# Kernel optimization log

Hardware: AMD Instinct MI355X
Metric: run time of the kernel (lower is better)

The kernel has to match this reference:

```python
import jax, jax.numpy as jnp
import numpy as np

EMBED_DIM = 768
SCALE = float(np.sqrt(EMBED_DIM / 9.0))


def setup_inputs() -> dict:
    key = jax.random.key(0)
    ks = jax.random.split(key, 7)
    D = EMBED_DIM
    s = 1.0 / np.sqrt(D)
    x = jax.random.normal(ks[0], (8, 2048, D), dtype=jnp.float32)
    Wq = jax.random.uniform(ks[1], (D, D), jnp.float32, -s, s)
    bq = jax.random.uniform(ks[2], (D,), jnp.float32, -s, s)
    Wk = jax.random.uniform(ks[3], (D, D), jnp.float32, -s, s)
    bk = jax.random.uniform(ks[4], (D,), jnp.float32, -s, s)
    Wv = jax.random.uniform(ks[5], (D, D), jnp.float32, -s, s)
    bv = jax.random.uniform(ks[6], (D,), jnp.float32, -s, s)
    return {"x": x, "Wq": Wq, "bq": bq, "Wk": Wk, "bk": bk, "Wv": Wv, "bv": bv}


def reference(x, Wq, bq, Wk, bk, Wv, bv):
    # nn.Linear: y = x @ W^T + b
    Q = jnp.einsum('bnd,ed->bne', x, Wq) + bq
    K = jnp.einsum('bnd,ed->bne', x, Wk) + bk
    V = jnp.einsum('bnd,ed->bne', x, Wv) + bv
    scores = jnp.einsum('bqd,bkd->bqk', Q, K) / SCALE  # [B, Nq, Nk]
    # NOTE: softmax over the QUERY axis (dim=-2), per the original module
    weights = jax.nn.softmax(scores, axis=-2)
    out = jnp.einsum('bqk,bkd->bqd', weights, V)
    return out + x
```

## Files before the change

kernel.cpp:

```cpp
#include <hip/hip_runtime.h>
#include <stdint.h>

#define B_ 8
#define N_ 2048
#define D_ 768

typedef unsigned short u16;
typedef unsigned int u32;
typedef __attribute__((ext_vector_type(8))) short bf16x8;
typedef __attribute__((ext_vector_type(8))) unsigned short u16x8;
typedef __attribute__((ext_vector_type(4))) float f32x4;

static constexpr float INV_SCALE = 0.10825317547305482f;

__device__ __forceinline__ u16 f2bf(float f) {
  union { float f; unsigned u; } v; v.f = f;
  return (u16)((v.u + 0x7FFFu + ((v.u >> 16) & 1u)) >> 16);
}
__device__ __forceinline__ float bf2f(u16 h) {
  union { unsigned u; float f; } v; v.u = ((unsigned)h) << 16;
  return v.f;
}
__device__ __forceinline__ f32x4 mfma16(bf16x8 a, bf16x8 b, f32x4 c) {
  return __builtin_amdgcn_mfma_f32_16x16x32_bf16(a, b, c, 0, 0, 0);
}
__device__ __forceinline__ void gl_lds16(const void* g, void* l) {
  __builtin_amdgcn_global_load_lds(
      (const __attribute__((address_space(1))) u32*)g,
      (__attribute__((address_space(3))) u32*)l, 16, 0, 0);
}

__global__ __launch_bounds__(256) void cast_kernel(
    const float* __restrict__ x, const float* __restrict__ wq,
    const float* __restrict__ wk, const float* __restrict__ wv,
    u16* __restrict__ xb, u16* __restrict__ wqb,
    u16* __restrict__ wkb, u16* __restrict__ wvb) {
  const long NX = (long)B_ * N_ * D_;
  const long NW = (long)D_ * D_;
  long i = ((long)blockIdx.x * 256 + threadIdx.x) * 8;
  const float* src; u16* dst; long off;
  if (i < NX) { src = x; dst = xb; off = i; }
  else {
    long j = i - NX;
    int seg = (int)(j / NW);
    off = j - (long)seg * NW;
    src = seg == 0 ? wq : (seg == 1 ? wk : wv);
    dst = seg == 0 ? wqb : (seg == 1 ? wkb : wvb);
  }
  float4 a = *(const float4*)(src + off);
  float4 b = *(const float4*)(src + off + 4);
  u16x8 o;
  o[0]=f2bf(a.x); o[1]=f2bf(a.y); o[2]=f2bf(a.z); o[3]=f2bf(a.w);
  o[4]=f2bf(b.x); o[5]=f2bf(b.y); o[6]=f2bf(b.z); o[7]=f2bf(b.w);
  *(u16x8*)(dst + off) = o;
}

template<int NT, int NF>
__device__ __forceinline__ void gemm256(
    const u16* __restrict__ Ag, long lda,
    const u16* __restrict__ Bg, long ldb,
    f32x4 (&acc)[8][NF]) {
  __shared__ u16 Ab[2][16384];
  __shared__ u16 Bb[2][NF * 4096];
  const int t_ = threadIdx.x, l = t_ & 63, w = t_ >> 6;
  const int lr = l & 15, kq = l >> 4;
  const int wm = w >> 2, wn = w & 3;
  const int arow = wm * 128, brow = wn * (NF * 16);
  const int s_rowl = l >> 3;
  const int s_sl = (l & 7) ^ (l >> 3);
  auto STAGE_A = [&](u16* As, int kt) {
    #pragma unroll
    for (int j = 0; j < 4; ++j) {
      const int row = j * 64 + w * 8 + s_rowl;
      gl_lds16(Ag + (long)row * lda + kt * 64 + s_sl * 8,
               As + ((j * 8192 + w * 1024) >> 1));
    }
  };
  auto STAGE_B = [&](u16* Bs, int kt) {
    #pragma unroll
    for (int j = 0; j < NF; ++j) {
      const int row = j * 64 + w * 8 + s_rowl;
      gl_lds16(Bg + (long)row * ldb + kt * 64 + s_sl * 8,
               Bs + ((j * 8192 + w * 1024) >> 1));
    }
  };

#define TILE(XA, XB, YA, YB, kt, DOST)                                       \
  {                                                                          \
    if (DOST) {                                                              \
      STAGE_A(YA, (kt) + 1);                                                 \
      asm volatile("s_waitcnt vmcnt(4)" ::: "memory");                       \
    } else {                                                                 \
      asm volatile("s_waitcnt vmcnt(0)" ::: "memory");                       \
    }                                                                        \
    __builtin_amdgcn_s_barrier();                                            \
    asm volatile("" ::: "memory");                                           \
    bf16x8 bf[NF][2];                                                        \
    _Pragma("unroll")                                                        \
    for (int nf = 0; nf < NF; ++nf) {                                        \
      const int row = brow + nf * 16 + lr;                                   \
      _Pragma("unroll")                                                      \
      for (int ks = 0; ks < 2; ++ks)                                         \
        bf[nf][ks] = *(const bf16x8*)(XB + row * 64 +                        \
                        (((4 * ks + kq) ^ (lr & 7)) * 8));                   \
    }                                                                        \
    {                                                                        \
      bf16x8 af[4][2];                                                       \
      _Pragma("unroll")                                                      \
      for (int mf = 0; mf < 4; ++mf) {                                       \
        const int row = arow + mf * 16 + lr;                                 \
        _Pragma("unroll")                                                    \
        for (int ks = 0; ks < 2; ++ks)                                       \
          af[mf][ks] = *(const bf16x8*)(XA + row * 64 +                      \
                          (((4 * ks + kq) ^ (lr & 7)) * 8));                 \
      }                                                                      \
      __builtin_amdgcn_s_setprio(1);                                         \
      _Pragma("unroll")                                                      \
      for (int ks = 0; ks < 2; ++ks)                                         \
        _Pragma("unroll")                                                    \
        for (int mf = 0; mf < 4; ++mf)                                       \
          _Pragma("unroll")                                                  \
          for (int nf = 0; nf < NF; ++nf)                                    \
            acc[mf][nf] = mfma16(af[mf][ks], bf[nf][ks], acc[mf][nf]);       \
      __builtin_amdgcn_s_setprio(0);                                         \
    }                                                                        \
    if (DOST) STAGE_B(YB, (kt) + 1);                                         \
    {                                                                        \
      bf16x8 af[4][2];                                                       \
      _Pragma("unroll")                                                      \
      for (int mf = 0; mf < 4; ++mf) {                                       \
        const int row = arow + 64 + mf * 16 + lr;                            \
        _Pragma("unroll")                                                    \
        for (int ks = 0; ks < 2; ++ks)                                       \
          af[mf][ks] = *(const bf16x8*)(XA + row * 64 +                      \
                          (((4 * ks + kq) ^ (lr & 7)) * 8));                 \
      }                                                                      \
      __builtin_amdgcn_s_setprio(1);                                         \
      _Pragma("unroll")                                                      \
      for (int ks = 0; ks < 2; ++ks)                                         \
        _Pragma("unroll")                                                    \
        for (int mf = 0; mf < 4; ++mf)                                       \
          _Pragma("unroll")                                                  \
          for (int nf = 0; nf < NF; ++nf)                                    \
            acc[4 + mf][nf] = mfma16(af[mf][ks], bf[nf][ks], acc[4 + mf][nf]); \
      __builtin_amdgcn_s_setprio(0);                                         \
    }                                                                        \
    asm volatile("" ::: "memory");                                           \
    __builtin_amdgcn_s_barrier();                                            \
  }

  STAGE_A(Ab[0], 0);
  STAGE_B(Bb[0], 0);
  for (int t2 = 0; t2 < NT; t2 += 2) {
    TILE(Ab[0], Bb[0], Ab[1], Bb[1], t2, true)
    TILE(Ab[1], Bb[1], Ab[0], Bb[0], t2 + 1, (t2 + 2 < NT))
  }
#undef TILE
}

__global__ __launch_bounds__(512, 1) void qkv_gemm(
    const u16* __restrict__ xb,
    const u16* __restrict__ wq, const u16* __restrict__ wk, const u16* __restrict__ wv,
    const float* __restrict__ bq, const float* __restrict__ bk, const float* __restrict__ bv,
    u16* __restrict__ Qs, u16* __restrict__ Kb, u16* __restrict__ Vb) {
  const int lin = blockIdx.x;
  const int xcd = lin & 7, inner = lin >> 3;
  const int rt = xcd * 8 + (inner & 7);
  const int ct = inner >> 3;
  const int mat = ct >> 2;
  const u16* W = mat == 0 ? wq : (mat == 1 ? wk : wv);
  const float* bias = mat == 0 ? bq : (mat == 1 ? bk : bv);
  u16* out = mat == 0 ? Qs : (mat == 1 ? Kb : Vb);
  const float scl = mat == 0 ? INV_SCALE : 1.0f;
  const int rbase = rt * 256, cbase = (ct & 3) * 192;

  f32x4 acc[8][3] = {};
  gemm256<D_ / 64, 3>(xb + (long)rbase * D_, D_, W + (long)cbase * D_, D_, acc);

  const int l = threadIdx.x & 63, w = threadIdx.x >> 6;
  const int lr = l & 15, orow = (l >> 4) * 4;
  const int wm = w >> 2, wn = w & 3;
  #pragma unroll
  for (int mf = 0; mf < 8; ++mf)
    #pragma unroll
    for (int nf = 0; nf < 3; ++nf) {
      int col = cbase + wn * 48 + nf * 16 + lr;
      float bc = bias[col];
      #pragma unroll
      for (int r = 0; r < 4; ++r) {
        int row = rbase + wm * 128 + mf * 16 + orow + r;
        out[(long)row * D_ + col] = f2bf((acc[mf][nf][r] + bc) * scl);
      }
    }
}

__global__ __launch_bounds__(512, 1) void qk_exp(
    const u16* __restrict__ Qs, const u16* __restrict__ Kb,
    u16* __restrict__ P, float* __restrict__ denpart) {
  const int lin = blockIdx.x;
  const int b = lin & 7, inner = lin >> 3;
  const int kblk = inner & 7, qblk = inner >> 3;

  f32x4 acc[8][4] = {};
  gemm256<D_ / 64, 4>(Qs + ((long)b * N_ + qblk * 256) * D_, D_,
                      Kb + ((long)b * N_ + kblk * 256) * D_, D_, acc);

  const int tt = threadIdx.x, l = tt & 63, w = tt >> 6;
  const int lr = l & 15, orow = (l >> 4) * 4;
  const int wm = w >> 2, wn = w & 3;
  float csum[4] = {0.f, 0.f, 0.f, 0.f};
  #pragma unroll
  for (int mf = 0; mf < 8; ++mf)
    #pragma unroll
    for (int nf = 0; nf < 4; ++nf) {
      long kk = kblk * 256 + wn * 64 + nf * 16 + lr;
      #pragma unroll
      for (int r = 0; r < 4; ++r) {
        long q = qblk * 256 + wm * 128 + mf * 16 + orow + r;
        float e = __expf(acc[mf][nf][r]);
        u16 pe = f2bf(e);
        P[((long)b * N_ + q) * N_ + kk] = pe;
        csum[nf] += bf2f(pe);
      }
    }
  #pragma unroll
  for (int nf = 0; nf < 4; ++nf) {
    csum[nf] += __shfl_xor(csum[nf], 16);
    csum[nf] += __shfl_xor(csum[nf], 32);
  }
  if (l < 16) {
    #pragma unroll
    for (int nf = 0; nf < 4; ++nf)
      denpart[((long)(qblk * 2 + wm) * B_ + b) * N_ +
              kblk * 256 + wn * 64 + nf * 16 + l] = csum[nf];
  }
}

__global__ __launch_bounds__(256) void scale_transpose(
    const u16* __restrict__ Vb, const float* __restrict__ denpart,
    u16* __restrict__ VsT) {
  const int b = blockIdx.z, k0 = blockIdx.y * 64, d0 = blockIdx.x * 64;
  __shared__ float tile[64][65];
  __shared__ float invden[64];
  const int t = threadIdx.x;
  if (t < 64) {
    float s = 0.f;
    for (int qs = 0; qs < 16; ++qs)
      s += denpart[((long)qs * B_ + b) * N_ + k0 + t];
    invden[t] = 1.0f / s;
  }
  __syncthreads();
  #pragma unroll
  for (int h = 0; h < 2; ++h) {
    const int kl = (t >> 3) + h * 32;
    const int d8 = (t & 7) * 8;
    bf16x8 v = *(const bf16x8*)(Vb + ((long)b * N_ + k0 + kl) * D_ + d0 + d8);
    const float s = invden[kl];
    #pragma unroll
    for (int j = 0; j < 8; ++j)
      tile[d8 + j][kl] = bf2f((u16)v[j]) * s;
  }
  __syncthreads();
  #pragma unroll
  for (int h = 0; h < 2; ++h) {
    const int dl = (t >> 3) + h * 32;
    const int k8 = (t & 7) * 8;
    u16x8 o;
    #pragma unroll
    for (int j = 0; j < 8; ++j)
      o[j] = f2bf(tile[dl][k8 + j]);
    *(u16x8*)(VsT + ((long)b * D_ + d0 + dl) * N_ + k0 + k8) = o;
  }
}

__global__ __launch_bounds__(512, 1) void pv_gemm(
    const u16* __restrict__ P, const u16* __restrict__ VsT,
    const u16* __restrict__ xb, float* __restrict__ out) {
  const int lin = blockIdx.x;
  const int b = lin & 7, inner = lin >> 3;
  const int qt = inner & 7, dt = inner >> 3;
  const int q0 = qt * 256, d0 = dt * 192;

  f32x4 acc[8][3] = {};
  gemm256<N_ / 64, 3>(P + ((long)b * N_ + q0) * N_, N_,
                      VsT + ((long)b * D_ + d0) * N_, N_, acc);

  const int l = threadIdx.x & 63, w = threadIdx.x >> 6;
  const int lr = l & 15, orow = (l >> 4) * 4;
  const int wm = w >> 2, wn = w & 3;
  #pragma unroll
  for (int mf = 0; mf < 8; ++mf)
    #pragma unroll
    for (int nf = 0; nf < 3; ++nf) {
      int dd = d0 + wn * 48 + nf * 16 + lr;
      #pragma unroll
      for (int r = 0; r < 4; ++r) {
        int q = q0 + wm * 128 + mf * 16 + orow + r;
        long idx = ((long)b * N_ + q) * D_ + dd;
        out[idx] = acc[mf][nf][r] + bf2f(xb[idx]);
      }
    }
}

extern "C" void kernel_launch(void* const* d_in, const int* in_sizes, int n_in,
                              void* d_out, int out_size, void* d_ws, size_t ws_size,
                              hipStream_t stream) {
  const float* x  = (const float*)d_in[0];
  const float* Wq = (const float*)d_in[1];
  const float* bq = (const float*)d_in[2];
  const float* Wk = (const float*)d_in[3];
  const float* bk = (const float*)d_in[4];
  const float* Wv = (const float*)d_in[5];
  const float* bv = (const float*)d_in[6];

  char* ws = (char*)d_ws;
  u16* xb  = (u16*)(ws + 0);
  u16* wqb = (u16*)(ws + 25165824);
  u16* wkb = (u16*)(ws + 26345472);
  u16* wvb = (u16*)(ws + 27525120);
  u16* Qs  = (u16*)(ws + 28704768);
  u16* Kb  = (u16*)(ws + 53870592);
  u16* Vb  = (u16*)(ws + 79036416);
  u16* VsT = (u16*)(ws + 104202240);
  u16* P   = (u16*)(ws + 129368064);
  float* denpart = (float*)(ws + 196476928);
  (void)in_sizes; (void)n_in; (void)out_size; (void)ws_size;

  cast_kernel<<<7008, 256, 0, stream>>>(x, Wq, Wk, Wv, xb, wqb, wkb, wvb);
  qkv_gemm<<<768, 512, 0, stream>>>(xb, wqb, wkb, wvb, bq, bk, bv, Qs, Kb, Vb);
  qk_exp<<<512, 512, 0, stream>>>(Qs, Kb, P, denpart);
  scale_transpose<<<dim3(12, 32, 8), 256, 0, stream>>>(Vb, denpart, VsT);
  pv_gemm<<<256, 512, 0, stream>>>(P, VsT, xb, (float*)d_out);
}
```

Before: 207.2 us.

## Halve GEMM M-tile to 128 rows and raise occupancy across all GEMM kernels

Replaces the 256-row block GEMM helper with a 128-row variant and doubles the grid sizes of the QKV, QK-exp and PV kernels. Launch bounds move from 1 to 4 blocks per CU, so each CU can hold more waves to hide latency and the grids fill the device better. The qk_exp kernel now reduces the two wave-row partial column sums in shared memory before writing, so denpart keeps 16 q-slices per column. The cost is less data reuse per block (more global/L2 traffic per FLOP) and tighter register limits that could cause spilling.

```diff
diff --git a/kernel.cpp b/kernel.cpp
--- a/kernel.cpp
+++ b/kernel.cpp
@@ -55,22 +55,22 @@
   *(u16x8*)(dst + off) = o;
 }
 
-template<int NT, int NF>
-__device__ __forceinline__ void gemm256(
+template<int NT, int NFB>
+__device__ __forceinline__ void gemm128(
     const u16* __restrict__ Ag, long lda,
     const u16* __restrict__ Bg, long ldb,
-    f32x4 (&acc)[8][NF]) {
-  __shared__ u16 Ab[2][16384];
-  __shared__ u16 Bb[2][NF * 4096];
+    f32x4 (&acc)[4][NFB]) {
+  __shared__ u16 Ab[2][8192];
+  __shared__ u16 Bb[2][NFB * 4096];
   const int t_ = threadIdx.x, l = t_ & 63, w = t_ >> 6;
   const int lr = l & 15, kq = l >> 4;
   const int wm = w >> 2, wn = w & 3;
-  const int arow = wm * 128, brow = wn * (NF * 16);
+  const int arow = wm * 64, brow = wn * (NFB * 16);
   const int s_rowl = l >> 3;
   const int s_sl = (l & 7) ^ (l >> 3);
   auto STAGE_A = [&](u16* As, int kt) {
     #pragma unroll
-    for (int j = 0; j < 4; ++j) {
+    for (int j = 0; j < 2; ++j) {
       const int row = j * 64 + w * 8 + s_rowl;
       gl_lds16(Ag + (long)row * lda + kt * 64 + s_sl * 8,
                As + ((j * 8192 + w * 1024) >> 1));
@@ -78,7 +78,7 @@
   };
   auto STAGE_B = [&](u16* Bs, int kt) {
     #pragma unroll
-    for (int j = 0; j < NF; ++j) {
+    for (int j = 0; j < NFB; ++j) {
       const int row = j * 64 + w * 8 + s_rowl;
       gl_lds16(Bg + (long)row * ldb + kt * 64 + s_sl * 8,
                Bs + ((j * 8192 + w * 1024) >> 1));
@@ -89,15 +89,15 @@
   {                                                                          \
     if (DOST) {                                                              \
       STAGE_A(YA, (kt) + 1);                                                 \
-      asm volatile("s_waitcnt vmcnt(4)" ::: "memory");                       \
+      asm volatile("s_waitcnt vmcnt(2)" ::: "memory");                       \
     } else {                                                                 \
       asm volatile("s_waitcnt vmcnt(0)" ::: "memory");                       \
     }                                                                        \
     __builtin_amdgcn_s_barrier();                                            \
     asm volatile("" ::: "memory");                                           \
-    bf16x8 bf[NF][2];                                                        \
+    bf16x8 bf[NFB][2];                                                       \
     _Pragma("unroll")                                                        \
-    for (int nf = 0; nf < NF; ++nf) {                                        \
+    for (int nf = 0; nf < NFB; ++nf) {                                       \
       const int row = brow + nf * 16 + lr;                                   \
       _Pragma("unroll")                                                      \
       for (int ks = 0; ks < 2; ++ks)                                         \
@@ -105,9 +105,9 @@
                         (((4 * ks + kq) ^ (lr & 7)) * 8));                   \
     }                                                                        \
     {                                                                        \
-      bf16x8 af[4][2];                                                       \
-      _Pragma("unroll")                                                      \
-      for (int mf = 0; mf < 4; ++mf) {                                       \
+      bf16x8 af[2][2];                                                       \
+      _Pragma("unroll")                                                      \
+      for (int mf = 0; mf < 2; ++mf) {                                       \
         const int row = arow + mf * 16 + lr;                                 \
         _Pragma("unroll")                                                    \
         for (int ks = 0; ks < 2; ++ks)                                       \
@@ -118,18 +118,18 @@
       _Pragma("unroll")                                                      \
       for (int ks = 0; ks < 2; ++ks)                                         \
         _Pragma("unroll")                                                    \
-        for (int mf = 0; mf < 4; ++mf)                                       \
+        for (int mf = 0; mf < 2; ++mf)                                       \
           _Pragma("unroll")                                                  \
-          for (int nf = 0; nf < NF; ++nf)                                    \
+          for (int nf = 0; nf < NFB; ++nf)                                   \
             acc[mf][nf] = mfma16(af[mf][ks], bf[nf][ks], acc[mf][nf]);       \
       __builtin_amdgcn_s_setprio(0);                                         \
     }                                                                        \
     if (DOST) STAGE_B(YB, (kt) + 1);                                         \
     {                                                                        \
-      bf16x8 af[4][2];                                                       \
-      _Pragma("unroll")                                                      \
-      for (int mf = 0; mf < 4; ++mf) {                                       \
-        const int row = arow + 64 + mf * 16 + lr;                            \
+      bf16x8 af[2][2];                                                       \
+      _Pragma("unroll")                                                      \
+      for (int mf = 0; mf < 2; ++mf) {                                       \
+        const int row = arow + 32 + mf * 16 + lr;                            \
         _Pragma("unroll")                                                    \
         for (int ks = 0; ks < 2; ++ks)                                       \
           af[mf][ks] = *(const bf16x8*)(XA + row * 64 +                      \
@@ -139,10 +139,10 @@
       _Pragma("unroll")                                                      \
       for (int ks = 0; ks < 2; ++ks)                                         \
         _Pragma("unroll")                                                    \
-        for (int mf = 0; mf < 4; ++mf)                                       \
+        for (int mf = 0; mf < 2; ++mf)                                       \
           _Pragma("unroll")                                                  \
-          for (int nf = 0; nf < NF; ++nf)                                    \
-            acc[4 + mf][nf] = mfma16(af[mf][ks], bf[nf][ks], acc[4 + mf][nf]); \
+          for (int nf = 0; nf < NFB; ++nf)                                   \
+            acc[2 + mf][nf] = mfma16(af[mf][ks], bf[nf][ks], acc[2 + mf][nf]); \
       __builtin_amdgcn_s_setprio(0);                                         \
     }                                                                        \
     asm volatile("" ::: "memory");                                           \
@@ -158,65 +158,66 @@
 #undef TILE
 }
 
-__global__ __launch_bounds__(512, 1) void qkv_gemm(
+__global__ __launch_bounds__(512, 4) void qkv_gemm(
     const u16* __restrict__ xb,
     const u16* __restrict__ wq, const u16* __restrict__ wk, const u16* __restrict__ wv,
     const float* __restrict__ bq, const float* __restrict__ bk, const float* __restrict__ bv,
     u16* __restrict__ Qs, u16* __restrict__ Kb, u16* __restrict__ Vb) {
   const int lin = blockIdx.x;
   const int xcd = lin & 7, inner = lin >> 3;
-  const int rt = xcd * 8 + (inner & 7);
-  const int ct = inner >> 3;
+  const int rt = xcd * 16 + (inner & 15);
+  const int ct = inner >> 4;
   const int mat = ct >> 2;
   const u16* W = mat == 0 ? wq : (mat == 1 ? wk : wv);
   const float* bias = mat == 0 ? bq : (mat == 1 ? bk : bv);
   u16* out = mat == 0 ? Qs : (mat == 1 ? Kb : Vb);
   const float scl = mat == 0 ? INV_SCALE : 1.0f;
-  const int rbase = rt * 256, cbase = (ct & 3) * 192;
-
-  f32x4 acc[8][3] = {};
-  gemm256<D_ / 64, 3>(xb + (long)rbase * D_, D_, W + (long)cbase * D_, D_, acc);
+  const int rbase = rt * 128, cbase = (ct & 3) * 192;
+
+  f32x4 acc[4][3] = {};
+  gemm128<D_ / 64, 3>(xb + (long)rbase * D_, D_, W + (long)cbase * D_, D_, acc);
 
   const int l = threadIdx.x & 63, w = threadIdx.x >> 6;
   const int lr = l & 15, orow = (l >> 4) * 4;
   const int wm = w >> 2, wn = w & 3;
   #pragma unroll
-  for (int mf = 0; mf < 8; ++mf)
+  for (int mf = 0; mf < 4; ++mf)
     #pragma unroll
     for (int nf = 0; nf < 3; ++nf) {
       int col = cbase + wn * 48 + nf * 16 + lr;
       float bc = bias[col];
       #pragma unroll
       for (int r = 0; r < 4; ++r) {
-        int row = rbase + wm * 128 + mf * 16 + orow + r;
+        int row = rbase + wm * 64 + mf * 16 + orow + r;
         out[(long)row * D_ + col] = f2bf((acc[mf][nf][r] + bc) * scl);
       }
     }
 }
 
-__global__ __launch_bounds__(512, 1) void qk_exp(
+__global__ __launch_bounds__(512, 4) void qk_exp(
     const u16* __restrict__ Qs, const u16* __restrict__ Kb,
     u16* __restrict__ P, float* __restrict__ denpart) {
+  __shared__ float dl[2][128];
   const int lin = blockIdx.x;
   const int b = lin & 7, inner = lin >> 3;
-  const int kblk = inner & 7, qblk = inner >> 3;
-
-  f32x4 acc[8][4] = {};
-  gemm256<D_ / 64, 4>(Qs + ((long)b * N_ + qblk * 256) * D_, D_,
-                      Kb + ((long)b * N_ + kblk * 256) * D_, D_, acc);
+  const int kblk = inner & 15, qblk = inner >> 4;
+
+  f32x4 acc[4][2] = {};
+  gemm128<D_ / 64, 2>(Qs + ((long)b * N_ + qblk * 128) * D_, D_,
+                      Kb + ((long)b * N_ + kblk * 128) * D_, D_, acc);
 
   const int tt = threadIdx.x, l = tt & 63, w = tt >> 6;
   const int lr = l & 15, orow = (l >> 4) * 4;
   const int wm = w >> 2, wn = w & 3;
-  float csum[4] = {0.f, 0.f, 0.f, 0.f};
-  #pragma unroll
-  for (int mf = 0; mf < 8; ++mf)
-    #pragma unroll
-    for (int nf = 0; nf < 4; ++nf) {
-      long kk = kblk * 256 + wn * 64 + nf * 16 + lr;
+  float csum[2] = {0.f, 0.f};
+  #pragma unroll
+  for (int mf = 0; mf < 4; ++mf)
+    #pragma unroll
+    for (int nf = 0; nf < 2; ++nf) {
+      long kk = kblk * 128 + wn * 32 + nf * 16 + lr;
       #pragma unroll
       for (int r = 0; r < 4; ++r) {
-        long q = qblk * 256 + wm * 128 + mf * 16 + orow + r;
+        long q = qblk * 128 + wm * 64 + mf * 16 + orow + r;
         float e = __expf(acc[mf][nf][r]);
         u16 pe = f2bf(e);
         P[((long)b * N_ + q) * N_ + kk] = pe;
@@ -224,16 +225,18 @@
       }
     }
   #pragma unroll
-  for (int nf = 0; nf < 4; ++nf) {
+  for (int nf = 0; nf < 2; ++nf) {
     csum[nf] += __shfl_xor(csum[nf], 16);
     csum[nf] += __shfl_xor(csum[nf], 32);
   }
   if (l < 16) {
     #pragma unroll
-    for (int nf = 0; nf < 4; ++nf)
-      denpart[((long)(qblk * 2 + wm) * B_ + b) * N_ +
-              kblk * 256 + wn * 64 + nf * 16 + l] = csum[nf];
-  }
+    for (int nf = 0; nf < 2; ++nf)
+      dl[wm][wn * 32 + nf * 16 + l] = csum[nf];
+  }
+  __syncthreads();
+  if (tt < 128)
+    denpart[((long)qblk * B_ + b) * N_ + kblk * 128 + tt] = dl[0][tt] + dl[1][tt];
 }
 
 __global__ __launch_bounds__(256) void scale_transpose(
@@ -273,29 +276,29 @@
   }
 }
 
-__global__ __launch_bounds__(512, 1) void pv_gemm(
+__global__ __launch_bounds__(512, 4) void pv_gemm(
     const u16* __restrict__ P, const u16* __restrict__ VsT,
     const u16* __restrict__ xb, float* __restrict__ out) {
   const int lin = blockIdx.x;
   const int b = lin & 7, inner = lin >> 3;
-  const int qt = inner & 7, dt = inner >> 3;
-  const int q0 = qt * 256, d0 = dt * 192;
-
-  f32x4 acc[8][3] = {};
-  gemm256<N_ / 64, 3>(P + ((long)b * N_ + q0) * N_, N_,
+  const int qt = inner & 15, dt = inner >> 4;
+  const int q0 = qt * 128, d0 = dt * 192;
+
+  f32x4 acc[4][3] = {};
+  gemm128<N_ / 64, 3>(P + ((long)b * N_ + q0) * N_, N_,
                       VsT + ((long)b * D_ + d0) * N_, N_, acc);
 
   const int l = threadIdx.x & 63, w = threadIdx.x >> 6;
   const int lr = l & 15, orow = (l >> 4) * 4;
   const int wm = w >> 2, wn = w & 3;
   #pragma unroll
-  for (int mf = 0; mf < 8; ++mf)
+  for (int mf = 0; mf < 4; ++mf)
     #pragma unroll
     for (int nf = 0; nf < 3; ++nf) {
       int dd = d0 + wn * 48 + nf * 16 + lr;
       #pragma unroll
       for (int r = 0; r < 4; ++r) {
-        int q = q0 + wm * 128 + mf * 16 + orow + r;
+        int q = q0 + wm * 64 + mf * 16 + orow + r;
         long idx = ((long)b * N_ + q) * D_ + dd;
         out[idx] = acc[mf][nf][r] + bf2f(xb[idx]);
       }
@@ -327,8 +330,8 @@
   (void)in_sizes; (void)n_in; (void)out_size; (void)ws_size;
 
   cast_kernel<<<7008, 256, 0, stream>>>(x, Wq, Wk, Wv, xb, wqb, wkb, wvb);
-  qkv_gemm<<<768, 512, 0, stream>>>(xb, wqb, wkb, wvb, bq, bk, bv, Qs, Kb, Vb);
-  qk_exp<<<512, 512, 0, stream>>>(Qs, Kb, P, denpart);
+  qkv_gemm<<<1536, 512, 0, stream>>>(xb, wqb, wkb, wvb, bq, bk, bv, Qs, Kb, Vb);
+  qk_exp<<<2048, 512, 0, stream>>>(Qs, Kb, P, denpart);
   scale_transpose<<<dim3(12, 32, 8), 256, 0, stream>>>(Vb, denpart, VsT);
-  pv_gemm<<<256, 512, 0, stream>>>(P, VsT, xb, (float*)d_out);
-}
+  pv_gemm<<<512, 512, 0, stream>>>(P, VsT, xb, (float*)d_out);
+}
```

Result: faster. 198.0 us (-4.5%).
